# Kernel tuning notes

Hardware: AMD Instinct MI355X
Metric: run time of the kernel (lower is better)

The kernel has to match this reference:

```python
import math
import jax, jax.numpy as jnp
import numpy as np


def conv2d(x, w, b=None, stride=(1, 1), padding=(1, 1)):
    # x: [N, C, H, W], w: [O, I, kh, kw]
    y = jax.lax.conv_general_dilated(
        x, w, window_strides=tuple(stride),
        padding=[(padding[0], padding[0]), (padding[1], padding[1])],
        dimension_numbers=('NCHW', 'OIHW', 'NCHW'))
    if b is not None:
        y = y + b[None, :, None, None]
    return y


def layernorm_chw(x, g, b, eps=1e-5):
    # x: [B, T, C, H, W]; normalize over last 3 dims (nn.LayerNorm([C,H,W]))
    m = jnp.mean(x, axis=(-3, -2, -1), keepdims=True)
    v = jnp.var(x, axis=(-3, -2, -1), keepdims=True)
    return (x - m) * jax.lax.rsqrt(v + eps) * g + b


def new_gelu(x):
    # NewGELU: tanh approximation
    c = math.sqrt(2.0 / math.pi)
    return 0.5 * x * (1.0 + jnp.tanh(c * (x + 0.044715 * x * x * x)))


def setup_inputs() -> dict:
    key = jax.random.key(0)
    ks = jax.random.split(key, 8)
    B, T, C, H, W = 4, 32, 32, 64, 64
    C_out, mixer = 32, 128
    s = 0.05
    return {
        'x': jax.random.normal(ks[0], (B, T, C, H, W), jnp.float32),
        'n1_g': jnp.ones((C, H, W), jnp.float32),
        'n1_b': jnp.zeros((C, H, W), jnp.float32),
        'n2_g': jnp.ones((C_out, H, W), jnp.float32),
        'n2_b': jnp.zeros((C_out, H, W), jnp.float32),
        'Wk': s * jax.random.normal(ks[1], (C_out, C, 3, 3), jnp.float32),
        'Wq': s * jax.random.normal(ks[2], (C_out, C, 3, 3), jnp.float32),
        'Wv': s * jax.random.normal(ks[3], (C_out, C, 3, 3), jnp.float32),
        'Wo': s * jax.random.normal(ks[4], (C_out, C_out, 3, 3), jnp.float32),
        'bo': jnp.zeros((C_out,), jnp.float32),
        'Wm1': s * jax.random.normal(ks[5], (mixer, C_out, 3, 3), jnp.float32),
        'bm1': jnp.zeros((mixer,), jnp.float32),
        'Wm2': s * jax.random.normal(ks[6], (C_out, mixer, 3, 3), jnp.float32),
        'bm2': jnp.zeros((C_out,), jnp.float32),
    }


def reference(x, n1_g, n1_b, n2_g, n2_b, Wk, Wq, Wv, Wo, bo, Wm1, bm1, Wm2, bm2):
    B, T, C, H, W = x.shape
    n_head = 8
    C_out = Wv.shape[0]
    hd = C_out // n_head

    # --- pre-norm + temporal CNN attention ---
    xn = layernorm_chw(x, n1_g, n1_b)
    xf = xn.reshape(B * T, C, H, W)
    k = conv2d(xf, Wk, stride=(2, 2))  # [BT, C_out, H', W'] (stride_t)
    q = conv2d(xf, Wq, stride=(2, 2))
    v = conv2d(xf, Wv)                 # [BT, C_out, H, W]
    Hp, Wp = k.shape[-2], k.shape[-1]

    # view(B, T, n_head, hd*H'*W').transpose(1, 2)
    k = k.reshape(B, T, n_head, hd * Hp * Wp).transpose(0, 2, 1, 3)
    q = q.reshape(B, T, n_head, hd * Hp * Wp).transpose(0, 2, 1, 3)
    v = v.reshape(B, T, n_head, hd * H * W).transpose(0, 2, 1, 3)

    scale = 1.0 / math.sqrt(hd * Hp * Wp)
    att = jnp.einsum('bhtd,bhsd->bhts', q, k) * scale  # [B, H, T, T]
    att = jax.nn.softmax(att, axis=-1)
    y = jnp.einsum('bhts,bhsd->bhtd', att, v)          # [B, H, T, hd*H*W]

    y = y.transpose(0, 2, 1, 3).reshape(B * T, C_out, H, W)
    y = conv2d(y, Wo, bo)  # attention output projection
    x = x + y.reshape(B, T, C_out, H, W)  # input_proj is Identity (C_in==C_out)

    # --- pre-norm + conv-GELU-conv mixer ---
    xn2 = layernorm_chw(x, n2_g, n2_b).reshape(B * T, C_out, H, W)
    h = new_gelu(conv2d(xn2, Wm1, bm1))
    h = conv2d(h, Wm2, bm2)
    x = x + h.reshape(B, T, C_out, H, W)
    return x
```

## Files before the change

### kernel.cpp

```cpp
#include <hip/hip_runtime.h>
#include <hip/hip_bf16.h>

using bf16 = __hip_bfloat16;
typedef short bf16x8 __attribute__((ext_vector_type(8)));
typedef float f32x4 __attribute__((ext_vector_type(4)));

#define AS1 __attribute__((address_space(1)))
#define AS3 __attribute__((address_space(3)))

__device__ inline float b2f(bf16 h) { return __bfloat162float(h); }
__device__ inline bf16 f2b(float f) { return __float2bfloat16(f); }
__device__ inline unsigned short f2bu(float f) {
    bf16 h = __float2bfloat16(f);
    unsigned short u;
    __builtin_memcpy(&u, &h, 2);
    return u;
}
__device__ inline float su2f(unsigned short u) {
    unsigned v = ((unsigned)u) << 16;
    return __uint_as_float(v);
}
__device__ inline void gload16(const bf16* gp, short* lp) {
    __builtin_amdgcn_global_load_lds((const AS1 void*)gp, (AS3 void*)lp, 16, 0, 0);
}
__device__ inline float fast_rcp(float a) {
#if __has_builtin(__builtin_amdgcn_rcpf)
    return __builtin_amdgcn_rcpf(a);
#else
    return 1.0f / a;
#endif
}
__device__ inline float gelu_new(float x) {
    float x3 = x * x * x;
    float z = -2.3022082f * __builtin_fmaf(0.044715f, x3, x);
    float e = exp2f(z);
    return x * fast_rcp(1.0f + e);
}
__device__ inline float2 ln_stats(const float2* spart, int sample) {
    float s = 0.f, ss = 0.f;
#pragma unroll
    for (int j = 0; j < 8; ++j) {
        float2 v = spart[sample * 8 + j];
        s += v.x; ss += v.y;
    }
    float m = s * (1.f / 131072.f);
    float var = ss * (1.f / 131072.f) - m * m;
    return make_float2(m, rsqrtf(var + 1e-5f));
}

__device__ inline void pack_one(const float* w, bf16* wpk, int i,
                                int CO, int CI, int CO_TOTAL, int co_off) {
    int tap = i % 9;
    int ci = (i / 9) % CI;
    int co = i / (9 * CI);
    wpk[((size_t)tap * CO_TOTAL + co_off + co) * CI + ci] = f2b(w[i]);
}
__global__ __launch_bounds__(256) void setup_all(const float* __restrict__ Wk,
                                                 const float* __restrict__ Wq,
                                                 const float* __restrict__ Wv,
                                                 const float* __restrict__ Wo,
                                                 const float* __restrict__ Wm1,
                                                 const float* __restrict__ Wm2,
                                                 const float* __restrict__ n2g,
                                                 const float* __restrict__ n2b,
                                                 bf16* __restrict__ wpk_kq,
                                                 bf16* __restrict__ wpk_v,
                                                 bf16* __restrict__ wpk_o,
                                                 bf16* __restrict__ wpk_m1,
                                                 bf16* __restrict__ wpk_m2,
                                                 float* __restrict__ gt,
                                                 float* __restrict__ bt,
                                                 float* __restrict__ zp) {
    int i = blockIdx.x * 256 + threadIdx.x;
    if (i < 9216)            pack_one(Wk, wpk_kq, i, 32, 32, 64, 0);
    else if (i < 18432)      pack_one(Wq, wpk_kq, i - 9216, 32, 32, 64, 32);
    else if (i < 27648)      pack_one(Wv, wpk_v, i - 18432, 32, 32, 32, 0);
    else if (i < 36864)      pack_one(Wo, wpk_o, i - 27648, 32, 32, 32, 0);
    else if (i < 73728)      pack_one(Wm1, wpk_m1, i - 36864, 128, 32, 128, 0);
    else if (i < 110592)     pack_one(Wm2, wpk_m2, i - 73728, 32, 128, 32, 0);
    else if (i < 110656)     zp[i - 110592] = 0.f;
    else if (i < 372800) {
        int j = i - 110656;
        int sel = j >> 17;
        int o = j & 131071;
        int p = o >> 5, c = o & 31;
        int src = c * 4096 + p;
        if (sel == 0) gt[o] = n2g[src];
        else          bt[o] = n2b[src];
    }
}

__global__ __launch_bounds__(256) void ln_part_f32(const float* __restrict__ xin,
                                                   float2* __restrict__ spart) {
    const int tid = threadIdx.x;
    const int sample = blockIdx.y, seg = blockIdx.x;
    const size_t base = (size_t)sample * 131072 + seg * 16384;
    float sum = 0.f, ss = 0.f;
    const float4* p = (const float4*)(xin + base);
    for (int l = 0; l < 16; ++l) {
        float4 v = p[l * 256 + tid];
        sum += v.x + v.y + v.z + v.w;
        ss += v.x * v.x + v.y * v.y + v.z * v.z + v.w * v.w;
    }
    __shared__ float rs[256], rs2[256];
    rs[tid] = sum; rs2[tid] = ss;
    __syncthreads();
    for (int off = 128; off > 0; off >>= 1) {
        if (tid < off) { rs[tid] += rs[tid + off]; rs2[tid] += rs2[tid + off]; }
        __syncthreads();
    }
    if (tid == 0) spart[sample * 8 + seg] = make_float2(rs[0], rs2[0]);
}

__global__ __launch_bounds__(256) void ln1_norm_t(const float* __restrict__ x,
                                                  const float* __restrict__ g,
                                                  const float* __restrict__ bb,
                                                  const float2* __restrict__ spart,
                                                  bf16* __restrict__ out) {
    __shared__ float tile[32][129];
    const int tid = threadIdx.x;
    const int sample = blockIdx.y;
    const int p0 = blockIdx.x * 128;
    float2 st = ln_stats(spart, sample);
    const float m = st.x, r = st.y;
    const size_t xb = (size_t)sample * 131072;
    for (int k = 0; k < 16; ++k) {
        int idx = k * 256 + tid;
        int c = idx >> 7, p = idx & 127;
        int gi = c * 4096 + p0 + p;
        float v = x[xb + gi];
        tile[c][p] = (v - m) * r * g[gi] + bb[gi];
    }
    __syncthreads();
    for (int k = 0; k < 8; ++k) {
        int idx = k * 256 + tid;
        int p = idx >> 4, c2 = (idx & 15) * 2;
        unsigned lo = (unsigned)f2bu(tile[c2][p]);
        unsigned hi = (unsigned)f2bu(tile[c2 + 1][p]);
        *(unsigned*)&out[xb + (size_t)(p0 + p) * 32 + c2] = lo | (hi << 16);
    }
}

__global__ __launch_bounds__(256) void ln2_norm(const bf16* __restrict__ xin,
                                                const float* __restrict__ gt,
                                                const float* __restrict__ bt,
                                                const float2* __restrict__ spart,
                                                bf16* __restrict__ out) {
    const int tid = threadIdx.x;
    const int sample = blockIdx.y;
    float2 st = ln_stats(spart, sample);
    const float m = st.x, r = st.y;
    int i0 = (blockIdx.x * 256 + tid) * 8;
    const size_t base = (size_t)sample * 131072 + i0;
    uint4 u = *(const uint4*)&xin[base];
    float4 g0 = *(const float4*)&gt[i0];
    float4 g1 = *(const float4*)&gt[i0 + 4];
    float4 b0 = *(const float4*)&bt[i0];
    float4 b1 = *(const float4*)&bt[i0 + 4];
    unsigned w[4] = {u.x, u.y, u.z, u.w};
    float gv[8] = {g0.x, g0.y, g0.z, g0.w, g1.x, g1.y, g1.z, g1.w};
    float bv[8] = {b0.x, b0.y, b0.z, b0.w, b1.x, b1.y, b1.z, b1.w};
    unsigned o[4];
#pragma unroll
    for (int j = 0; j < 4; ++j) {
        float lo = __uint_as_float(w[j] << 16);
        float hi = __uint_as_float(w[j] & 0xffff0000u);
        lo = (lo - m) * r * gv[2 * j] + bv[2 * j];
        hi = (hi - m) * r * gv[2 * j + 1] + bv[2 * j + 1];
        o[j] = (unsigned)f2bu(lo) | ((unsigned)f2bu(hi) << 16);
    }
    uint4 st4 = make_uint4(o[0], o[1], o[2], o[3]);
    *(uint4*)&out[base] = st4;
}

template <int CI, int CO_TOTAL, int CO_BLK, int EPI, int ROWS>
__device__ __forceinline__ void conv_body(char* pool,
                                          const bf16* __restrict__ in,
                                          const bf16* __restrict__ wpk,
                                          const float* __restrict__ bias,
                                          const void* __restrict__ res,
                                          void* __restrict__ out,
                                          const bf16* __restrict__ zpage,
                                          float2* __restrict__ spart_out,
                                          int in_s0, int out_s0,
                                          int ng, int cg, int smp) {
    constexpr int CHUNKS = CI / 32;
    constexpr int MT = CO_BLK / 16;
    constexpr int NT = ROWS * 64;
    constexpr int HR = ROWS + 2;
    constexpr int IN_ITEMS = HR * 66 * 4;
    constexpr int IN_PAD = ((IN_ITEMS + 63) / 64) * 64;
    constexpr int IN_ITERS = (IN_PAD + NT - 1) / NT;
    constexpr int W_ITEMS = 9 * CO_BLK * 4;
    constexpr int W_ITERS = (W_ITEMS + NT - 1) / NT;

    short* s_in = (short*)pool;
    short* s_w = (short*)(pool + (size_t)IN_PAD * 16);
    float* rsum = (float*)(pool + (size_t)IN_PAD * 16 + 9 * CO_BLK * 64);
    float* rss = rsum + NT;

    const int tid = threadIdx.x;
    const int lane = tid & 63;
    const int wv = tid >> 6;
    const int quad = lane >> 4;
    const int n16 = lane & 15;
    const int co0 = cg * CO_BLK;
    const int y0 = ng * ROWS;

    const size_t in_base = (size_t)(in_s0 + smp) * 4096 * CI;

    int gin[IN_ITERS];
#pragma unroll
    for (int it = 0; it < IN_ITERS; ++it) {
        int i = it * NT + tid;
        int sub = i & 3;
        int x = (i >> 2) % 66;
        int row = i / 264;
        int y = y0 + row - 1;
        int xg = x - 1;
        bool ok = (i < IN_ITEMS) && (y >= 0) && (y < 64) && (xg >= 0) && (xg < 64);
        int grp = sub ^ (x & 3) ^ ((x >> 2) & 1);
        gin[it] = ok ? ((y * 64 + xg) * CI + grp * 8) : -1;
    }
    int gw[W_ITERS];
#pragma unroll
    for (int it = 0; it < W_ITERS; ++it) {
        int i = it * NT + tid;
        if (i < W_ITEMS) {
            int sub = i & 3;
            int co = (i >> 2) % CO_BLK;
            int tap = i / (CO_BLK * 4);
            int grp = sub ^ (co & 3) ^ ((co >> 2) & 1);
            gw[it] = (tap * CO_TOTAL + co0 + co) * CI + grp * 8;
        } else gw[it] = 0;
    }

    f32x4 acc[MT][4];
#pragma unroll
    for (int mt = 0; mt < MT; ++mt)
#pragma unroll
        for (int j = 0; j < 4; ++j) acc[mt][j] = (f32x4){0.f, 0.f, 0.f, 0.f};

    for (int chunk = 0; chunk < CHUNKS; ++chunk) {
        const int ci0 = chunk * 32;
        __syncthreads();
#pragma unroll
        for (int it = 0; it < IN_ITERS; ++it) {
            int i0 = it * NT + (tid & ~63);
            if (i0 < IN_PAD) {
                const bf16* gp = (gin[it] >= 0) ? (in + in_base + gin[it] + ci0) : zpage;
                gload16(gp, s_in + (size_t)i0 * 8);
            }
        }
#pragma unroll
        for (int it = 0; it < W_ITERS; ++it) {
            int i0 = it * NT + (tid & ~63);
            if (i0 < W_ITEMS) {
                const bf16* gp = wpk + gw[it] + ci0;
                gload16(gp, s_w + (size_t)i0 * 8);
            }
        }
        __syncthreads();

#pragma unroll
        for (int ky = 0; ky < 3; ++ky) {
#pragma unroll
            for (int kx = 0; kx < 3; ++kx) {
                const int tap = ky * 3 + kx;
                bf16x8 bfrag[4];
#pragma unroll
                for (int j = 0; j < 4; ++j) {
                    int x = j * 16 + n16 + kx;
                    int ps = quad ^ (x & 3) ^ ((x >> 2) & 1);
                    bfrag[j] = *(const bf16x8*)&s_in[((wv + ky) * 66 + x) * 32 + ps * 8];
                }
#pragma unroll
                for (int mt = 0; mt < MT; ++mt) {
                    int mrow = mt * 16 + n16;
                    int ps = quad ^ (mrow & 3) ^ ((mrow >> 2) & 1);
                    bf16x8 afrag = *(const bf16x8*)&s_w[(tap * CO_BLK + mrow) * 32 + ps * 8];
#pragma unroll
                    for (int j = 0; j < 4; ++j)
                        acc[mt][j] = __builtin_amdgcn_mfma_f32_16x16x32_bf16(afrag, bfrag[j], acc[mt][j], 0, 0, 0);
                }
            }
        }
    }

    const int osmp = out_s0 + smp;
    float lsum = 0.f, lss = 0.f;
#pragma unroll
    for (int j = 0; j < 4; ++j) {
        int pos = (y0 + wv) * 64 + j * 16 + n16;
#pragma unroll
        for (int mt = 0; mt < MT; ++mt) {
            int coutb = co0 + mt * 16 + quad * 4;
            float b0 = 0.f, b1 = 0.f, b2 = 0.f, b3 = 0.f;
            if constexpr (EPI != 1) {
                float4 bv = *(const float4*)&bias[coutb];
                b0 = bv.x; b1 = bv.y; b2 = bv.z; b3 = bv.w;
            }
            float v0 = acc[mt][j][0] + b0;
            float v1 = acc[mt][j][1] + b1;
            float v2 = acc[mt][j][2] + b2;
            float v3 = acc[mt][j][3] + b3;
            if constexpr (EPI == 1 || EPI == 2 || EPI == 3) {
                if constexpr (EPI == 2) {
                    const float* xr = (const float*)res + (size_t)osmp * 131072 + (size_t)coutb * 4096 + pos;
                    v0 += xr[0]; v1 += xr[4096]; v2 += xr[8192]; v3 += xr[12288];
                    lsum += v0 + v1 + v2 + v3;
                    lss += v0 * v0 + v1 * v1 + v2 * v2 + v3 * v3;
                } else if constexpr (EPI == 3) {
                    v0 = gelu_new(v0); v1 = gelu_new(v1); v2 = gelu_new(v2); v3 = gelu_new(v3);
                }
                ushort4 st;
                st.x = f2bu(v0); st.y = f2bu(v1); st.z = f2bu(v2); st.w = f2bu(v3);
                *(ushort4*)&((bf16*)out)[((size_t)osmp * 4096 + pos) * CO_TOTAL + coutb] = st;
            } else {
                ushort4 rv = *(const ushort4*)&((const bf16*)res)[((size_t)osmp * 4096 + pos) * 32 + coutb];
                v0 += su2f(rv.x); v1 += su2f(rv.y); v2 += su2f(rv.z); v3 += su2f(rv.w);
                float* op = (float*)out + (size_t)osmp * 131072 + (size_t)coutb * 4096 + pos;
                op[0] = v0; op[4096] = v1; op[8192] = v2; op[12288] = v3;
            }
        }
    }

    if constexpr (EPI == 2) {
        rsum[tid] = lsum; rss[tid] = lss;
        __syncthreads();
        for (int off = NT / 2; off > 0; off >>= 1) {
            if (tid < off) { rsum[tid] += rsum[tid + off]; rss[tid] += rss[tid + off]; }
            __syncthreads();
        }
        if (tid == 0) spart_out[smp * 8 + ng] = make_float2(rsum[0], rss[0]);
    }
}

template <int CI, int CO_TOTAL, int CO_BLK, int EPI, int ROWS = 8>
__global__ __launch_bounds__(ROWS * 64) void conv_lds(const bf16* __restrict__ in,
                                                      const bf16* __restrict__ wpk,
                                                      const float* __restrict__ bias,
                                                      const void* __restrict__ res,
                                                      void* __restrict__ out,
                                                      const bf16* __restrict__ zpage,
                                                      float2* __restrict__ spart_out,
                                                      int in_s0, int out_s0) {
    constexpr int NG = 64 / ROWS;
    constexpr int IN_PAD = ((((ROWS + 2) * 66 * 4) + 63) / 64) * 64;
    constexpr int POOL = IN_PAD * 16 + 9 * CO_BLK * 64 + (EPI == 2 ? ROWS * 64 * 8 : 0);
    __shared__ __align__(16) char pool[POOL];
    conv_body<CI, CO_TOTAL, CO_BLK, EPI, ROWS>(pool, in, wpk, bias, res, out, zpage,
                                               spart_out, in_s0, out_s0,
                                               blockIdx.x % NG, blockIdx.x / NG, blockIdx.y);
}

__global__ __launch_bounds__(512) void conv_kqv(const bf16* __restrict__ xn,
                                                const bf16* __restrict__ wpk_kq,
                                                const bf16* __restrict__ wpk_v,
                                                bf16* __restrict__ KQ,
                                                bf16* __restrict__ Vb,
                                                const bf16* __restrict__ zpage) {
    __shared__ __align__(16) char pool[61440];
    const int bx = blockIdx.x;
    const int smp = blockIdx.y;
    if (bx >= 2) {
        conv_body<32, 32, 32, 1, 8>(pool, xn, wpk_v, nullptr, nullptr, Vb, zpage,
                                    nullptr, 0, 0, bx - 2, 0, smp);
        return;
    }
    constexpr int PAD = 40;
    short* s_w = (short*)pool;
    const int tid = threadIdx.x;
    const int lane = tid & 63;
    const int wv = tid >> 6;
    const int quad = lane >> 4;
    const int n16 = lane & 15;
    const int ng = bx;

    f32x4 acc[4][4];
#pragma unroll
    for (int mt = 0; mt < 4; ++mt)
#pragma unroll
        for (int j = 0; j < 4; ++j) acc[mt][j] = (f32x4){0.f, 0.f, 0.f, 0.f};

    const size_t in_base = (size_t)smp * 4096 * 32;

    for (int idx = tid; idx < 4608; idx += 512) {
        int e = idx * 4;
        int tap = e / 2048;
        int rem = e - tap * 2048;
        int col = rem >> 5;
        int k = rem & 31;
        const ushort4 src = *(const ushort4*)&wpk_kq[((size_t)tap * 64 + col) * 32 + k];
        *(ushort4*)&s_w[(tap * 64 + col) * PAD + k] = src;
    }
    __syncthreads();

#pragma unroll
    for (int ky = 0; ky < 3; ++ky) {
#pragma unroll
        for (int kx = 0; kx < 3; ++kx) {
            const int tap = ky * 3 + kx;
            bf16x8 bfrag[4];
#pragma unroll
            for (int j = 0; j < 4; ++j) {
                int tile = ng * 32 + wv * 4 + j;
                int yo = tile >> 1;
                int xo = (tile & 1) * 16;
                int xi = (xo + n16) * 2 + kx - 1;
                int yi = yo * 2 + ky - 1;
                bool valid = (xi >= 0) && (xi < 64) && (yi >= 0) && (yi < 64);
                uint4 u;
                if (valid)
                    u = *(const uint4*)&xn[in_base + ((size_t)yi * 64 + xi) * 32 + quad * 8];
                else
                    u = make_uint4(0u, 0u, 0u, 0u);
                __builtin_memcpy(&bfrag[j], &u, 16);
            }
#pragma unroll
            for (int mt = 0; mt < 4; ++mt) {
                bf16x8 afrag = *(const bf16x8*)&s_w[(tap * 64 + mt * 16 + n16) * PAD + quad * 8];
#pragma unroll
                for (int j = 0; j < 4; ++j)
                    acc[mt][j] = __builtin_amdgcn_mfma_f32_16x16x32_bf16(afrag, bfrag[j], acc[mt][j], 0, 0, 0);
            }
        }
    }

#pragma unroll
    for (int j = 0; j < 4; ++j) {
        int tile = ng * 32 + wv * 4 + j;
        int yo = tile >> 1;
        int xo = (tile & 1) * 16;
        int pos = yo * 32 + xo + n16;
#pragma unroll
        for (int mt = 0; mt < 4; ++mt) {
            int coutb = mt * 16 + quad * 4;
            ushort4 st;
            st.x = f2bu(acc[mt][j][0]); st.y = f2bu(acc[mt][j][1]);
            st.z = f2bu(acc[mt][j][2]); st.w = f2bu(acc[mt][j][3]);
            *(ushort4*)&KQ[((size_t)smp * 1024 + pos) * 64 + coutb] = st;
        }
    }
}

__global__ __launch_bounds__(256) void attn_scores_mfma(const bf16* __restrict__ KQ,
                                                        bf16* __restrict__ att) {
    __shared__ float red[4][32][33];
    __shared__ float sc[32][33];
    const int tid = threadIdx.x;
    const int lane = tid & 63;
    const int wv = tid >> 6;
    const int quad = lane >> 4;
    const int n16 = lane & 15;
    const int h = blockIdx.x & 7;
    const int b = blockIdx.x >> 3;
    const size_t base = (size_t)b * 32 * 65536 + (size_t)h * 4;

    f32x4 acc[2][2];
#pragma unroll
    for (int mt = 0; mt < 2; ++mt)
#pragma unroll
        for (int nt = 0; nt < 2; ++nt) acc[mt][nt] = (f32x4){0.f, 0.f, 0.f, 0.f};

    for (int kc = 0; kc < 32; ++kc) {
        const int p0 = wv * 256 + kc * 8 + quad * 2;
        bf16x8 afrag[2], bfrag[2];
#pragma unroll
        for (int mt = 0; mt < 2; ++mt) {
            const bf16* qp = &KQ[base + 32 + (size_t)(mt * 16 + n16) * 65536 + (size_t)p0 * 64];
            uint2 lo = *(const uint2*)qp;
            uint2 hi = *(const uint2*)(qp + 64);
            uint4 u = make_uint4(lo.x, lo.y, hi.x, hi.y);
            __builtin_memcpy(&afrag[mt], &u, 16);
        }
#pragma unroll
        for (int nt = 0; nt < 2; ++nt) {
            const bf16* kp = &KQ[base + (size_t)(nt * 16 + n16) * 65536 + (size_t)p0 * 64];
            uint2 lo = *(const uint2*)kp;
            uint2 hi = *(const uint2*)(kp + 64);
            uint4 u = make_uint4(lo.x, lo.y, hi.x, hi.y);
            __builtin_memcpy(&bfrag[nt], &u, 16);
        }
#pragma unroll
        for (int mt = 0; mt < 2; ++mt)
#pragma unroll
            for (int nt = 0; nt < 2; ++nt)
                acc[mt][nt] = __builtin_amdgcn_mfma_f32_16x16x32_bf16(afrag[mt], bfrag[nt], acc[mt][nt], 0, 0, 0);
    }
#pragma unroll
    for (int mt = 0; mt < 2; ++mt)
#pragma unroll
        for (int nt = 0; nt < 2; ++nt)
#pragma unroll
            for (int r = 0; r < 4; ++r)
                red[wv][mt * 16 + quad * 4 + r][nt * 16 + n16] = acc[mt][nt][r];
    __syncthreads();
    for (int i = tid; i < 1024; i += 256) {
        int t = i >> 5, s = i & 31;
        sc[t][s] = (red[0][t][s] + red[1][t][s] + red[2][t][s] + red[3][t][s]) * (1.0f / 64.0f);
    }
    __syncthreads();
    if (tid < 32) {
        float mx = -1e30f;
        for (int s2 = 0; s2 < 32; ++s2) mx = fmaxf(mx, sc[tid][s2]);
        float sum = 0.f;
        for (int s2 = 0; s2 < 32; ++s2) sum += expf(sc[tid][s2] - mx);
        float inv = 1.f / sum;
        bf16* arow = &att[((size_t)blockIdx.x * 32 + tid) * 32];
        for (int s2 = 0; s2 < 32; ++s2) arow[s2] = f2b(expf(sc[tid][s2] - mx) * inv);
    }
}

__global__ __launch_bounds__(256) void attn_apply_mfma(const bf16* __restrict__ att,
                                                       const bf16* __restrict__ V,
                                                       bf16* __restrict__ Y) {
    __shared__ short vlds[512 * 40];
    __shared__ short ylds[32 * 512];
    const int tid = threadIdx.x;
    const int lane = tid & 63;
    const int wv = tid >> 6;
    const int quad = lane >> 4;
    const int n16 = lane & 15;
    const int pb = blockIdx.x;
    const int b = blockIdx.y;

    for (int l = 0; l < 8; ++l) {
        int u = l * 256 + tid;
        int s = u >> 6;
        int col8 = (u & 63) * 8;
        uint4 v = *(const uint4*)&V[(((size_t)(b * 32 + s) * 4096 + pb * 16) * 32) + col8];
        unsigned short us[8];
        __builtin_memcpy(us, &v, 16);
#pragma unroll
        for (int j = 0; j < 8; ++j) {
            int idx = col8 + j;
            int p = idx >> 5, c = idx & 31;
            int row = ((c >> 2) * 16 + p) * 4 + (c & 3);
            vlds[row * 40 + s] = (short)us[j];
        }
    }
    __syncthreads();

    const int e = wv * 16 + n16;
    const int p = e >> 2, cl = e & 3;
    for (int h = 0; h < 8; ++h) {
        bf16x8 bfrag = *(const bf16x8*)&vlds[(h * 64 + e) * 40 + quad * 8];
        const int c = h * 4 + cl;
#pragma unroll
        for (int mt = 0; mt < 2; ++mt) {
            bf16x8 afrag = *(const bf16x8*)&att[((size_t)(b * 8 + h) * 32 + mt * 16 + n16) * 32 + quad * 8];
            f32x4 d = __builtin_amdgcn_mfma_f32_16x16x32_bf16(afrag, bfrag,
                                                              (f32x4){0.f, 0.f, 0.f, 0.f}, 0, 0, 0);
#pragma unroll
            for (int r = 0; r < 4; ++r) {
                int t = mt * 16 + quad * 4 + r;
                ylds[t * 512 + p * 32 + c] = (short)f2bu(d[r]);
            }
        }
    }
    __syncthreads();

    for (int l = 0; l < 8; ++l) {
        int u = l * 256 + tid;
        int t = u >> 6;
        int col8 = (u & 63) * 8;
        *(uint4*)&Y[(((size_t)(b * 32 + t) * 4096 + pb * 16) * 32) + col8] =
            *(const uint4*)&ylds[t * 512 + col8];
    }
}

extern "C" void kernel_launch(void* const* d_in, const int* in_sizes, int n_in,
                              void* d_out, int out_size, void* d_ws, size_t ws_size,
                              hipStream_t stream) {
    const float* x   = (const float*)d_in[0];
    const float* n1g = (const float*)d_in[1];
    const float* n1b = (const float*)d_in[2];
    const float* n2g = (const float*)d_in[3];
    const float* n2b = (const float*)d_in[4];
    const float* Wk  = (const float*)d_in[5];
    const float* Wq  = (const float*)d_in[6];
    const float* Wv  = (const float*)d_in[7];
    const float* Wo  = (const float*)d_in[8];
    const float* bo  = (const float*)d_in[9];
    const float* Wm1 = (const float*)d_in[10];
    const float* bm1 = (const float*)d_in[11];
    const float* Wm2 = (const float*)d_in[12];
    const float* bm2 = (const float*)d_in[13];

    char* ws = (char*)d_ws;
    const size_t A_OFF = 0;
    const size_t B_OFF = 33554432;
    const size_t D_OFF = 67108864;
    const size_t E_OFF = 67239936;
    const size_t F_OFF = 67461120;
    const size_t C_OFF = 68519936;

    bf16*  xn   = (bf16*)(ws + A_OFF);
    bf16*  Yb   = (bf16*)(ws + A_OFF);
    bf16*  xn2  = (bf16*)(ws + A_OFF);
    bf16*  Vb   = (bf16*)(ws + B_OFF);
    bf16*  X1   = (bf16*)(ws + B_OFF);
    bf16*  attbf = (bf16*)(ws + D_OFF);
    bf16*  wpk_kq = (bf16*)(ws + E_OFF);
    bf16*  wpk_v  = (bf16*)(ws + E_OFF + 36864);
    bf16*  wpk_o  = (bf16*)(ws + E_OFF + 55296);
    bf16*  wpk_m1 = (bf16*)(ws + E_OFF + 73728);
    bf16*  wpk_m2 = (bf16*)(ws + E_OFF + 147456);
    float* g2t  = (float*)(ws + F_OFF);
    float* b2t  = (float*)(ws + F_OFF + 524288);
    float2* spart = (float2*)(ws + F_OFF + 1048576);
    bf16*  zpg  = (bf16*)(ws + F_OFF + 1057792);
    bf16*  KQb  = (bf16*)(ws + C_OFF);
    bf16*  Hb   = (bf16*)(ws + C_OFF);

    const size_t HB_PER_SAMPLE = 1048576;
    int chunk = 128;
    if (ws_size < C_OFF + 128 * HB_PER_SAMPLE) {
        size_t avail = (ws_size > C_OFF) ? (ws_size - C_OFF) : HB_PER_SAMPLE;
        chunk = (int)(avail / HB_PER_SAMPLE);
        if (chunk < 1) chunk = 1;
        if (chunk > 128) chunk = 128;
    }

    setup_all<<<1457, 256, 0, stream>>>(Wk, Wq, Wv, Wo, Wm1, Wm2, n2g, n2b,
                                        wpk_kq, wpk_v, wpk_o, wpk_m1, wpk_m2,
                                        g2t, b2t, (float*)zpg);
    ln_part_f32<<<dim3(8, 128), 256, 0, stream>>>(x, spart);
    ln1_norm_t<<<dim3(32, 128), 256, 0, stream>>>(x, n1g, n1b, spart, xn);
    conv_kqv<<<dim3(10, 128), 512, 0, stream>>>(xn, wpk_kq, wpk_v, KQb, Vb, zpg);
    attn_scores_mfma<<<32, 256, 0, stream>>>(KQb, attbf);
    attn_apply_mfma<<<dim3(256, 4), 256, 0, stream>>>(attbf, Vb, Yb);
    conv_lds<32, 32, 32, 2, 8><<<dim3(8, 128), 512, 0, stream>>>(Yb, wpk_o, bo, x, X1, zpg, spart, 0, 0);
    ln2_norm<<<dim3(64, 128), 256, 0, stream>>>(X1, g2t, b2t, spart, xn2);
    for (int s0 = 0; s0 < 128; s0 += chunk) {
        int n = (128 - s0 < chunk) ? (128 - s0) : chunk;
        conv_lds<32, 128, 64, 3, 8><<<dim3(16, n), 512, 0, stream>>>(xn2, wpk_m1, bm1, nullptr, Hb, zpg, nullptr, s0, 0);
        conv_lds<128, 32, 32, 4, 8><<<dim3(8, n), 512, 0, stream>>>(Hb, wpk_m2, bm2, X1, (float*)d_out, zpg, nullptr, 0, s0);
    }
}
```

Before: 450.4 us.

## Split attention score reduction across blocks and swizzle conv block IDs per XCD

The attention-score kernel ran only 32 blocks, each summing over the whole 8192-long feature dimension. It is now split into 8 segments per (batch, head), 256 blocks in total, which write fp32 partial scores to workspace. A new small kernel sums the partials and applies softmax. Separately, the conv kernels remap their flat block ID so that consecutive logical blocks land on the same XCD, aiming at better L2 locality. The cost is an extra launch plus an fp32 partial buffer round trip.

```diff
diff --git a/kernel.cpp b/kernel.cpp
--- a/kernel.cpp
+++ b/kernel.cpp
@@ -46,6 +46,12 @@
     float m = s * (1.f / 131072.f);
     float var = ss * (1.f / 131072.f) - m * m;
     return make_float2(m, rsqrtf(var + 1e-5f));
+}
+__device__ inline int xcd_swz_id() {
+    int bid = blockIdx.y * gridDim.x + blockIdx.x;
+    int nwg = gridDim.x * gridDim.y;
+    if ((nwg & 7) == 0) return (bid & 7) * (nwg >> 3) + (bid >> 3);
+    return bid;
 }
 
 __device__ inline void pack_one(const float* w, bf16* wpk, int i,
@@ -349,9 +355,12 @@
     constexpr int IN_PAD = ((((ROWS + 2) * 66 * 4) + 63) / 64) * 64;
     constexpr int POOL = IN_PAD * 16 + 9 * CO_BLK * 64 + (EPI == 2 ? ROWS * 64 * 8 : 0);
     __shared__ __align__(16) char pool[POOL];
+    int l = xcd_swz_id();
+    int bx = l % gridDim.x;
+    int smp = l / gridDim.x;
     conv_body<CI, CO_TOTAL, CO_BLK, EPI, ROWS>(pool, in, wpk, bias, res, out, zpage,
                                                spart_out, in_s0, out_s0,
-                                               blockIdx.x % NG, blockIdx.x / NG, blockIdx.y);
+                                               bx % NG, bx / NG, smp);
 }
 
 __global__ __launch_bounds__(512) void conv_kqv(const bf16* __restrict__ xn,
@@ -361,8 +370,9 @@
                                                 bf16* __restrict__ Vb,
                                                 const bf16* __restrict__ zpage) {
     __shared__ __align__(16) char pool[61440];
-    const int bx = blockIdx.x;
-    const int smp = blockIdx.y;
+    int l = xcd_swz_id();
+    const int bx = l % gridDim.x;
+    const int smp = l / gridDim.x;
     if (bx >= 2) {
         conv_body<32, 32, 32, 1, 8>(pool, xn, wpk_v, nullptr, nullptr, Vb, zpage,
                                     nullptr, 0, 0, bx - 2, 0, smp);
@@ -444,17 +454,18 @@
     }
 }
 
-__global__ __launch_bounds__(256) void attn_scores_mfma(const bf16* __restrict__ KQ,
-                                                        bf16* __restrict__ att) {
+__global__ __launch_bounds__(256) void attn_scores_part(const bf16* __restrict__ KQ,
+                                                        float* __restrict__ scpart) {
     __shared__ float red[4][32][33];
-    __shared__ float sc[32][33];
     const int tid = threadIdx.x;
     const int lane = tid & 63;
     const int wv = tid >> 6;
     const int quad = lane >> 4;
     const int n16 = lane & 15;
-    const int h = blockIdx.x & 7;
-    const int b = blockIdx.x >> 3;
+    const int seg = blockIdx.x;
+    const int bh = blockIdx.y;
+    const int h = bh & 7;
+    const int b = bh >> 3;
     const size_t base = (size_t)b * 32 * 65536 + (size_t)h * 4;
 
     f32x4 acc[2][2];
@@ -463,8 +474,8 @@
 #pragma unroll
         for (int nt = 0; nt < 2; ++nt) acc[mt][nt] = (f32x4){0.f, 0.f, 0.f, 0.f};
 
-    for (int kc = 0; kc < 32; ++kc) {
-        const int p0 = wv * 256 + kc * 8 + quad * 2;
+    for (int kc = 0; kc < 4; ++kc) {
+        const int p0 = seg * 128 + wv * 32 + kc * 8 + quad * 2;
         bf16x8 afrag[2], bfrag[2];
 #pragma unroll
         for (int mt = 0; mt < 2; ++mt) {
@@ -496,9 +507,24 @@
             for (int r = 0; r < 4; ++r)
                 red[wv][mt * 16 + quad * 4 + r][nt * 16 + n16] = acc[mt][nt][r];
     __syncthreads();
+    float* dst = scpart + ((size_t)bh * 8 + seg) * 1024;
     for (int i = tid; i < 1024; i += 256) {
         int t = i >> 5, s = i & 31;
-        sc[t][s] = (red[0][t][s] + red[1][t][s] + red[2][t][s] + red[3][t][s]) * (1.0f / 64.0f);
+        dst[i] = red[0][t][s] + red[1][t][s] + red[2][t][s] + red[3][t][s];
+    }
+}
+
+__global__ __launch_bounds__(256) void attn_soft(const float* __restrict__ scpart,
+                                                 bf16* __restrict__ att) {
+    __shared__ float sc[32][33];
+    const int tid = threadIdx.x;
+    const int bh = blockIdx.x;
+    const float* src = scpart + (size_t)bh * 8192;
+    for (int i = tid; i < 1024; i += 256) {
+        float v = 0.f;
+#pragma unroll
+        for (int g = 0; g < 8; ++g) v += src[g * 1024 + i];
+        sc[i >> 5][i & 31] = v * (1.0f / 64.0f);
     }
     __syncthreads();
     if (tid < 32) {
@@ -507,7 +533,7 @@
         float sum = 0.f;
         for (int s2 = 0; s2 < 32; ++s2) sum += expf(sc[tid][s2] - mx);
         float inv = 1.f / sum;
-        bf16* arow = &att[((size_t)blockIdx.x * 32 + tid) * 32];
+        bf16* arow = &att[((size_t)bh * 32 + tid) * 32];
         for (int s2 = 0; s2 < 32; ++s2) arow[s2] = f2b(expf(sc[tid][s2] - mx) * inv);
     }
 }
@@ -612,6 +638,7 @@
     float2* spart = (float2*)(ws + F_OFF + 1048576);
     bf16*  zpg  = (bf16*)(ws + F_OFF + 1057792);
     bf16*  KQb  = (bf16*)(ws + C_OFF);
+    float* scpart = (float*)(ws + C_OFF + 16777216);
     bf16*  Hb   = (bf16*)(ws + C_OFF);
 
     const size_t HB_PER_SAMPLE = 1048576;
@@ -629,7 +656,8 @@
     ln_part_f32<<<dim3(8, 128), 256, 0, stream>>>(x, spart);
     ln1_norm_t<<<dim3(32, 128), 256, 0, stream>>>(x, n1g, n1b, spart, xn);
     conv_kqv<<<dim3(10, 128), 512, 0, stream>>>(xn, wpk_kq, wpk_v, KQb, Vb, zpg);
-    attn_scores_mfma<<<32, 256, 0, stream>>>(KQb, attbf);
+    attn_scores_part<<<dim3(8, 32), 256, 0, stream>>>(KQb, scpart);
+    attn_soft<<<32, 256, 0, stream>>>(scpart, attbf);
     attn_apply_mfma<<<dim3(256, 4), 256, 0, stream>>>(attbf, Vb, Yb);
     conv_lds<32, 32, 32, 2, 8><<<dim3(8, 128), 512, 0, stream>>>(Yb, wpk_o, bo, x, X1, zpg, spart, 0, 0);
     ln2_norm<<<dim3(64, 128), 256, 0, stream>>>(X1, g2t, b2t, spart, xn2);
```

After: 406.0 us. 1.11x faster.
